# Kernel tuning notes

Measured on AMD Instinct MI355X. Metric: run time of the kernel, lower is better.

## Reference

```python
import jax, jax.numpy as jnp
import numpy as np
from jax import lax

WIN = 7          # win_size
K1 = 0.01
K2 = 0.03
NP_W = WIN * WIN
COV_NORM = NP_W / (NP_W - 1)


def _box_filter(x):
    w = jnp.ones((1, 1, WIN, WIN), x.dtype) / NP_W
    return lax.conv_general_dilated(
        x, w, window_strides=(1, 1), padding='VALID',
        dimension_numbers=('NCHW', 'OIHW', 'NCHW'))


def setup_inputs() -> dict:
    key = jax.random.key(0)
    k1, k2 = jax.random.split(key)
    B, C, T, H, W = 16, 1, 20, 256, 256
    Xt = jax.random.uniform(k1, (B, C, T, H, W), dtype=jnp.float32)
    Yt = jax.random.uniform(k2, (B, C, T, H, W), dtype=jnp.float32)
    data_range = jnp.ones((1,), dtype=jnp.float32)  # unused: overwritten per frame
    return {"Xt": Xt, "Yt": Yt, "data_range": data_range}


def reference(Xt, Yt, data_range):
    B, C, T, H, W = Xt.shape
    # Fold time into batch: frame index = b*T + t
    X = Xt.transpose(0, 2, 1, 3, 4).reshape(B * T, C, H, W)
    Y = Yt.transpose(0, 2, 1, 3, 4).reshape(B * T, C, H, W)

    # Per-frame data_range = max over the whole batch slice Yt[:,:,t]
    # (torch.Tensor([Y.max()]) detaches it from autograd in the original)
    dr = lax.stop_gradient(jnp.max(Yt, axis=(0, 1, 3, 4)))      # [T]
    dr = jnp.tile(dr, B)[:, None, None, None]                   # [B*T,1,1,1]
    C1 = (K1 * dr) ** 2
    C2 = (K2 * dr) ** 2

    # One conv call over 5 stacked moment maps
    stacked = jnp.concatenate([X, Y, X * X, Y * Y, X * Y], axis=0)
    filt = _box_filter(stacked)
    ux, uy, uxx, uyy, uxy = jnp.split(filt, 5, axis=0)

    vx = COV_NORM * (uxx - ux * ux)
    vy = COV_NORM * (uyy - uy * uy)
    vxy = COV_NORM * (uxy - ux * uy)

    A1 = 2 * ux * uy + C1
    A2 = 2 * vxy + C2
    B1 = ux * ux + uy * uy + C1
    B2 = vx + vy + C2
    S = (A1 * A2) / (B1 * B2)

    # sum_t (1 - mean(S_t)) / T == 1 - mean(S) since every frame has equal count
    return 1.0 - jnp.mean(S)
```

## Files before the change

### kernel.cpp

```cpp
#include <hip/hip_runtime.h>


#define HH 256
#define WW 256
#define OUTW 250
#define NT 20
#define NB 16
#define NFRAMES (NT * NB)
#define STRIPS 50
#define RPS 5
#define NWAVES (NFRAMES * STRIPS)
#define WPB 4
#define NBLK2 (NWAVES / WPB)
#define NXCD 8

__device__ __forceinline__ float wave_sum(float v) {
#pragma unroll
    for (int off = 32; off > 0; off >>= 1) v += __shfl_down(v, off, 64);
    return v;
}

__global__ __launch_bounds__(256) void dr_max_kernel(const float* __restrict__ Y,
                                                     float* __restrict__ dr_part) {
    int t = blockIdx.x;
    int bq = blockIdx.y;
    const float4* p = (const float4*)(Y + (size_t)((bq >> 2) * NT + t) * (HH * WW))
                      + (bq & 3) * 4096;
    float m = 0.f;
#pragma unroll 4
    for (int k = 0; k < 16; ++k) {
        float4 v = p[k * 256 + threadIdx.x];
        m = fmaxf(m, fmaxf(fmaxf(v.x, v.y), fmaxf(v.z, v.w)));
    }
#pragma unroll
    for (int off = 32; off > 0; off >>= 1) m = fmaxf(m, __shfl_down(m, off, 64));
    __shared__ float smax[4];
    int lane = threadIdx.x & 63, w = threadIdx.x >> 6;
    if (lane == 0) smax[w] = m;
    __syncthreads();
    if (threadIdx.x == 0)
        dr_part[t * 64 + bq] = fmaxf(fmaxf(smax[0], smax[1]), fmaxf(smax[2], smax[3]));
}


__device__ __forceinline__ float ssim_px(float hx, float hy, float hxx, float hyy,
                                         float hxy, float c1, float c2) {
    const float cov = 49.0f / 48.0f;
    float hx2 = hx * hx, hy2 = hy * hy, hxy1 = hx * hy;
    float A1 = __builtin_fmaf(2.f, hxy1, c1);
    float B1 = hx2 + hy2 + c1;
    float t1 = __builtin_fmaf(49.f, hxx, -hx2);
    float t2 = __builtin_fmaf(49.f, hyy, -hy2);
    float t3 = __builtin_fmaf(49.f, hxy, -hxy1);
    float A2 = __builtin_fmaf(2.f * cov, t3, c2);
    float B2 = __builtin_fmaf(cov, t1 + t2, c2);
    return (A1 * A2) * __builtin_amdgcn_rcpf(B1 * B2);
}

__device__ __forceinline__ float4 taps7_shfl(float4 s) {
    float P  = (s.x + s.y) + (s.z + s.w);
    float P1 = __shfl_down(P,   1, 64);
    float w1 = __shfl_down(s.w, 1, 64);
    float x2 = __shfl_down(s.x, 2, 64);
    float y2 = __shfl_down(s.y, 2, 64);
    float base = P + P1;
    float o0 = base - w1;
    float o1 = base - s.x;
    float o2 = s.z + s.w + P1 + x2;
    float o3 = o2 - s.z + y2;
    return make_float4(o0, o1, o2, o3);
}

__device__ __forceinline__ void slide5(float4& sx, float4& sy, float4& sxx,
                                       float4& syy, float4& sxy,
                                       float4 xo, float4 yo, float4 xn, float4 yn) {
    sx.x += xn.x - xo.x; sx.y += xn.y - xo.y; sx.z += xn.z - xo.z; sx.w += xn.w - xo.w;
    sy.x += yn.x - yo.x; sy.y += yn.y - yo.y; sy.z += yn.z - yo.z; sy.w += yn.w - yo.w;
    sxx.x += xn.x * xn.x - xo.x * xo.x; sxx.y += xn.y * xn.y - xo.y * xo.y;
    sxx.z += xn.z * xn.z - xo.z * xo.z; sxx.w += xn.w * xn.w - xo.w * xo.w;
    syy.x += yn.x * yn.x - yo.x * yo.x; syy.y += yn.y * yn.y - yo.y * yo.y;
    syy.z += yn.z * yn.z - yo.z * yo.z; syy.w += yn.w * yn.w - yo.w * yo.w;
    sxy.x += xn.x * yn.x - xo.x * yo.x; sxy.y += xn.y * yn.y - xo.y * yo.y;
    sxy.z += xn.z * yn.z - xo.z * yo.z; sxy.w += xn.w * yn.w - xo.w * yo.w;
}

__global__ __launch_bounds__(256, 4) void ssim_kernel(const float* __restrict__ X,
                                                      const float* __restrict__ Y,
                                                      const float* __restrict__ dr_part,
                                                      float* __restrict__ partials) {
    int w = threadIdx.x >> 6;
    int l = threadIdx.x & 63;
    int bid = blockIdx.x;
    int swz = (bid % NXCD) * (NBLK2 / NXCD) + bid / NXCD;
    int wid = swz * WPB + w;
    int frame = wid / STRIPS;
    int strip = wid % STRIPS;
    int t = frame % NT;
    const float4* x4 = (const float4*)(X + (size_t)frame * (HH * WW));
    const float4* y4 = (const float4*)(Y + (size_t)frame * (HH * WW));
    int c0 = 4 * l;

    float dr = dr_part[t * 64 + l];
#pragma unroll
    for (int off = 32; off > 0; off >>= 1) dr = fmaxf(dr, __shfl_xor(dr, off, 64));
    float c1 = 2401.f * (0.01f * dr) * (0.01f * dr);
    float c2 = 2401.f * (0.03f * dr) * (0.03f * dr);

    int r0 = strip * RPS;

    float4 sx = make_float4(0, 0, 0, 0), sy = sx, sxx = sx, syy = sx, sxy = sx;
#pragma unroll
    for (int dy = 0; dy < 7; ++dy) {
        float4 xv = x4[(r0 + dy) * 64 + l];
        float4 yv = y4[(r0 + dy) * 64 + l];
        sx.x += xv.x; sx.y += xv.y; sx.z += xv.z; sx.w += xv.w;
        sy.x += yv.x; sy.y += yv.y; sy.z += yv.z; sy.w += yv.w;
        sxx.x += xv.x * xv.x; sxx.y += xv.y * xv.y; sxx.z += xv.z * xv.z; sxx.w += xv.w * xv.w;
        syy.x += yv.x * yv.x; syy.y += yv.y * yv.y; syy.z += yv.z * yv.z; syy.w += yv.w * yv.w;
        sxy.x += xv.x * yv.x; sxy.y += xv.y * yv.y; sxy.z += xv.z * yv.z; sxy.w += xv.w * yv.w;
    }

    float acc = 0.f;
    for (int it = 0; it < RPS; ++it) {
        int r = r0 + it;
        bool last = (it == RPS - 1);

        float4 xo, yo, xn, yn;
        if (!last) {
            xo = x4[r * 64 + l];       yo = y4[r * 64 + l];
            xn = x4[(r + 7) * 64 + l]; yn = y4[(r + 7) * 64 + l];
        }

        float4 hx  = taps7_shfl(sx);
        float4 hy  = taps7_shfl(sy);
        float4 hxx = taps7_shfl(sxx);
        float4 hyy = taps7_shfl(syy);
        float4 hxy = taps7_shfl(sxy);

        if (c0 + 0 < OUTW) acc += ssim_px(hx.x, hy.x, hxx.x, hyy.x, hxy.x, c1, c2);
        if (c0 + 1 < OUTW) acc += ssim_px(hx.y, hy.y, hxx.y, hyy.y, hxy.y, c1, c2);
        if (c0 + 2 < OUTW) acc += ssim_px(hx.z, hy.z, hxx.z, hyy.z, hxy.z, c1, c2);
        if (c0 + 3 < OUTW) acc += ssim_px(hx.w, hy.w, hxx.w, hyy.w, hxy.w, c1, c2);

        if (!last)
            slide5(sx, sy, sxx, syy, sxy, xo, yo, xn, yn);
    }

    acc = wave_sum(acc);
    if (l == 0) partials[wid] = acc;
}

__global__ __launch_bounds__(256) void final_kernel(const float* __restrict__ partials,
                                                    float* __restrict__ out) {
    float s = 0.f;
    for (int i = threadIdx.x; i < NWAVES; i += 256) s += partials[i];
    s = wave_sum(s);
    __shared__ float ssum[4];
    int lane = threadIdx.x & 63, w = threadIdx.x >> 6;
    if (lane == 0) ssum[w] = s;
    __syncthreads();
    if (threadIdx.x == 0) {
        float total = ssum[0] + ssum[1] + ssum[2] + ssum[3];
        const double denom = (double)NFRAMES * OUTW * OUTW;
        out[0] = (float)(1.0 - (double)total / denom);
    }
}

extern "C" void kernel_launch(void* const* d_in, const int* in_sizes, int n_in,
                              void* d_out, int out_size, void* d_ws, size_t ws_size,
                              hipStream_t stream) {
    const float* X = (const float*)d_in[0];
    const float* Y = (const float*)d_in[1];

    float* ws = (float*)d_ws;
    float* dr_part  = ws;
    float* partials = ws + 2048;

    dim3 g1(NT, NB * 4);
    hipLaunchKernelGGL(dr_max_kernel, g1, dim3(256), 0, stream, Y, dr_part);
    hipLaunchKernelGGL(ssim_kernel, dim3(NBLK2), dim3(256), 0, stream,
                       X, Y, (const float*)dr_part, partials);
    hipLaunchKernelGGL(final_kernel, dim3(1), dim3(256), 0, stream,
                       partials, (float*)d_out);
}
```

Baseline: 210.5 us.

## Process two row strips per wave to raise ILP and halve waves

Each wave now handles two independent 5-row strips, interleaving their loads, shuffles and SSIM math so the instruction stream has more independent work to hide latency. The sliding-window update uses fma with (new-old)(new+old) for the squared moments, and per-block partial sums are reduced in shared memory before being written. This halves the number of waves launched and raises register pressure, which may reduce occupancy under the 4-block launch bound.

New measurement: 210.8 us. No clear change (+0.1%).

```diff
diff --git a/kernel.cpp b/kernel.cpp
--- a/kernel.cpp
+++ b/kernel.cpp
@@ -7,11 +7,11 @@
 #define NT 20
 #define NB 16
 #define NFRAMES (NT * NB)
-#define STRIPS 50
 #define RPS 5
-#define NWAVES (NFRAMES * STRIPS)
+#define PAIRS 25
+#define NPAIRW (NFRAMES * PAIRS)
 #define WPB 4
-#define NBLK2 (NWAVES / WPB)
+#define NBLK2 (NPAIRW / WPB)
 #define NXCD 8
 
 __device__ __forceinline__ float wave_sum(float v) {
@@ -74,14 +74,32 @@
 __device__ __forceinline__ void slide5(float4& sx, float4& sy, float4& sxx,
                                        float4& syy, float4& sxy,
                                        float4 xo, float4 yo, float4 xn, float4 yn) {
-    sx.x += xn.x - xo.x; sx.y += xn.y - xo.y; sx.z += xn.z - xo.z; sx.w += xn.w - xo.w;
-    sy.x += yn.x - yo.x; sy.y += yn.y - yo.y; sy.z += yn.z - yo.z; sy.w += yn.w - yo.w;
-    sxx.x += xn.x * xn.x - xo.x * xo.x; sxx.y += xn.y * xn.y - xo.y * xo.y;
-    sxx.z += xn.z * xn.z - xo.z * xo.z; sxx.w += xn.w * xn.w - xo.w * xo.w;
-    syy.x += yn.x * yn.x - yo.x * yo.x; syy.y += yn.y * yn.y - yo.y * yo.y;
-    syy.z += yn.z * yn.z - yo.z * yo.z; syy.w += yn.w * yn.w - yo.w * yo.w;
-    sxy.x += xn.x * yn.x - xo.x * yo.x; sxy.y += xn.y * yn.y - xo.y * yo.y;
-    sxy.z += xn.z * yn.z - xo.z * yo.z; sxy.w += xn.w * yn.w - xo.w * yo.w;
+    float dx, ex, dy, ey;
+    dx = xn.x - xo.x; ex = xn.x + xo.x; sx.x += dx; sxx.x = __builtin_fmaf(dx, ex, sxx.x);
+    dy = yn.x - yo.x; ey = yn.x + yo.x; sy.x += dy; syy.x = __builtin_fmaf(dy, ey, syy.x);
+    sxy.x += xn.x * yn.x - xo.x * yo.x;
+    dx = xn.y - xo.y; ex = xn.y + xo.y; sx.y += dx; sxx.y = __builtin_fmaf(dx, ex, sxx.y);
+    dy = yn.y - yo.y; ey = yn.y + yo.y; sy.y += dy; syy.y = __builtin_fmaf(dy, ey, syy.y);
+    sxy.y += xn.y * yn.y - xo.y * yo.y;
+    dx = xn.z - xo.z; ex = xn.z + xo.z; sx.z += dx; sxx.z = __builtin_fmaf(dx, ex, sxx.z);
+    dy = yn.z - yo.z; ey = yn.z + yo.z; sy.z += dy; syy.z = __builtin_fmaf(dy, ey, syy.z);
+    sxy.z += xn.z * yn.z - xo.z * yo.z;
+    dx = xn.w - xo.w; ex = xn.w + xo.w; sx.w += dx; sxx.w = __builtin_fmaf(dx, ex, sxx.w);
+    dy = yn.w - yo.w; ey = yn.w + yo.w; sy.w += dy; syy.w = __builtin_fmaf(dy, ey, syy.w);
+    sxy.w += xn.w * yn.w - xo.w * yo.w;
+}
+
+__device__ __forceinline__ void accum7(float4& sx, float4& sy, float4& sxx,
+                                       float4& syy, float4& sxy,
+                                       float4 xv, float4 yv) {
+    sx.x += xv.x; sx.y += xv.y; sx.z += xv.z; sx.w += xv.w;
+    sy.x += yv.x; sy.y += yv.y; sy.z += yv.z; sy.w += yv.w;
+    sxx.x = __builtin_fmaf(xv.x, xv.x, sxx.x); sxx.y = __builtin_fmaf(xv.y, xv.y, sxx.y);
+    sxx.z = __builtin_fmaf(xv.z, xv.z, sxx.z); sxx.w = __builtin_fmaf(xv.w, xv.w, sxx.w);
+    syy.x = __builtin_fmaf(yv.x, yv.x, syy.x); syy.y = __builtin_fmaf(yv.y, yv.y, syy.y);
+    syy.z = __builtin_fmaf(yv.z, yv.z, syy.z); syy.w = __builtin_fmaf(yv.w, yv.w, syy.w);
+    sxy.x = __builtin_fmaf(xv.x, yv.x, sxy.x); sxy.y = __builtin_fmaf(xv.y, yv.y, sxy.y);
+    sxy.z = __builtin_fmaf(xv.z, yv.z, sxy.z); sxy.w = __builtin_fmaf(xv.w, yv.w, sxy.w);
 }
 
 __global__ __launch_bounds__(256, 4) void ssim_kernel(const float* __restrict__ X,
@@ -93,8 +111,8 @@
     int bid = blockIdx.x;
     int swz = (bid % NXCD) * (NBLK2 / NXCD) + bid / NXCD;
     int wid = swz * WPB + w;
-    int frame = wid / STRIPS;
-    int strip = wid % STRIPS;
+    int frame = wid / PAIRS;
+    int pair  = wid % PAIRS;
     int t = frame % NT;
     const float4* x4 = (const float4*)(X + (size_t)frame * (HH * WW));
     const float4* y4 = (const float4*)(Y + (size_t)frame * (HH * WW));
@@ -106,54 +124,75 @@
     float c1 = 2401.f * (0.01f * dr) * (0.01f * dr);
     float c2 = 2401.f * (0.03f * dr) * (0.03f * dr);
 
-    int r0 = strip * RPS;
-
-    float4 sx = make_float4(0, 0, 0, 0), sy = sx, sxx = sx, syy = sx, sxy = sx;
+    int rA = pair * (2 * RPS);
+    int rB = rA + RPS;
+
+    float4 sxA = make_float4(0, 0, 0, 0), syA = sxA, sxxA = sxA, syyA = sxA, sxyA = sxA;
+    float4 sxB = sxA, syB = sxA, sxxB = sxA, syyB = sxA, sxyB = sxA;
 #pragma unroll
     for (int dy = 0; dy < 7; ++dy) {
-        float4 xv = x4[(r0 + dy) * 64 + l];
-        float4 yv = y4[(r0 + dy) * 64 + l];
-        sx.x += xv.x; sx.y += xv.y; sx.z += xv.z; sx.w += xv.w;
-        sy.x += yv.x; sy.y += yv.y; sy.z += yv.z; sy.w += yv.w;
-        sxx.x += xv.x * xv.x; sxx.y += xv.y * xv.y; sxx.z += xv.z * xv.z; sxx.w += xv.w * xv.w;
-        syy.x += yv.x * yv.x; syy.y += yv.y * yv.y; syy.z += yv.z * yv.z; syy.w += yv.w * yv.w;
-        sxy.x += xv.x * yv.x; sxy.y += xv.y * yv.y; sxy.z += xv.z * yv.z; sxy.w += xv.w * yv.w;
+        float4 xvA = x4[(rA + dy) * 64 + l];
+        float4 yvA = y4[(rA + dy) * 64 + l];
+        float4 xvB = x4[(rB + dy) * 64 + l];
+        float4 yvB = y4[(rB + dy) * 64 + l];
+        accum7(sxA, syA, sxxA, syyA, sxyA, xvA, yvA);
+        accum7(sxB, syB, sxxB, syyB, sxyB, xvB, yvB);
     }
 
     float acc = 0.f;
     for (int it = 0; it < RPS; ++it) {
-        int r = r0 + it;
         bool last = (it == RPS - 1);
 
-        float4 xo, yo, xn, yn;
+        float4 xoA, yoA, xnA, ynA, xoB, yoB, xnB, ynB;
         if (!last) {
-            xo = x4[r * 64 + l];       yo = y4[r * 64 + l];
-            xn = x4[(r + 7) * 64 + l]; yn = y4[(r + 7) * 64 + l];
-        }
-
-        float4 hx  = taps7_shfl(sx);
-        float4 hy  = taps7_shfl(sy);
-        float4 hxx = taps7_shfl(sxx);
-        float4 hyy = taps7_shfl(syy);
-        float4 hxy = taps7_shfl(sxy);
-
-        if (c0 + 0 < OUTW) acc += ssim_px(hx.x, hy.x, hxx.x, hyy.x, hxy.x, c1, c2);
-        if (c0 + 1 < OUTW) acc += ssim_px(hx.y, hy.y, hxx.y, hyy.y, hxy.y, c1, c2);
-        if (c0 + 2 < OUTW) acc += ssim_px(hx.z, hy.z, hxx.z, hyy.z, hxy.z, c1, c2);
-        if (c0 + 3 < OUTW) acc += ssim_px(hx.w, hy.w, hxx.w, hyy.w, hxy.w, c1, c2);
-
-        if (!last)
-            slide5(sx, sy, sxx, syy, sxy, xo, yo, xn, yn);
+            int ra = rA + it, rb = rB + it;
+            xoA = x4[ra * 64 + l];       yoA = y4[ra * 64 + l];
+            xnA = x4[(ra + 7) * 64 + l]; ynA = y4[(ra + 7) * 64 + l];
+            xoB = x4[rb * 64 + l];       yoB = y4[rb * 64 + l];
+            xnB = x4[(rb + 7) * 64 + l]; ynB = y4[(rb + 7) * 64 + l];
+        }
+
+        {
+            float4 hx  = taps7_shfl(sxA);
+            float4 hy  = taps7_shfl(syA);
+            float4 hxx = taps7_shfl(sxxA);
+            float4 hyy = taps7_shfl(syyA);
+            float4 hxy = taps7_shfl(sxyA);
+            if (c0 + 0 < OUTW) acc += ssim_px(hx.x, hy.x, hxx.x, hyy.x, hxy.x, c1, c2);
+            if (c0 + 1 < OUTW) acc += ssim_px(hx.y, hy.y, hxx.y, hyy.y, hxy.y, c1, c2);
+            if (c0 + 2 < OUTW) acc += ssim_px(hx.z, hy.z, hxx.z, hyy.z, hxy.z, c1, c2);
+            if (c0 + 3 < OUTW) acc += ssim_px(hx.w, hy.w, hxx.w, hyy.w, hxy.w, c1, c2);
+        }
+        {
+            float4 hx  = taps7_shfl(sxB);
+            float4 hy  = taps7_shfl(syB);
+            float4 hxx = taps7_shfl(sxxB);
+            float4 hyy = taps7_shfl(syyB);
+            float4 hxy = taps7_shfl(sxyB);
+            if (c0 + 0 < OUTW) acc += ssim_px(hx.x, hy.x, hxx.x, hyy.x, hxy.x, c1, c2);
+            if (c0 + 1 < OUTW) acc += ssim_px(hx.y, hy.y, hxx.y, hyy.y, hxy.y, c1, c2);
+            if (c0 + 2 < OUTW) acc += ssim_px(hx.z, hy.z, hxx.z, hyy.z, hxy.z, c1, c2);
+            if (c0 + 3 < OUTW) acc += ssim_px(hx.w, hy.w, hxx.w, hyy.w, hxy.w, c1, c2);
+        }
+
+        if (!last) {
+            slide5(sxA, syA, sxxA, syyA, sxyA, xoA, yoA, xnA, ynA);
+            slide5(sxB, syB, sxxB, syyB, sxyB, xoB, yoB, xnB, ynB);
+        }
     }
 
     acc = wave_sum(acc);
-    if (l == 0) partials[wid] = acc;
+    __shared__ float ssum[4];
+    if (l == 0) ssum[w] = acc;
+    __syncthreads();
+    if (threadIdx.x == 0)
+        partials[blockIdx.x] = (ssum[0] + ssum[1]) + (ssum[2] + ssum[3]);
 }
 
 __global__ __launch_bounds__(256) void final_kernel(const float* __restrict__ partials,
                                                     float* __restrict__ out) {
     float s = 0.f;
-    for (int i = threadIdx.x; i < NWAVES; i += 256) s += partials[i];
+    for (int i = threadIdx.x; i < NBLK2; i += 256) s += partials[i];
     s = wave_sum(s);
     __shared__ float ssum[4];
     int lane = threadIdx.x & 63, w = threadIdx.x >> 6;
```
